# Performance work log

Measured on AMD Instinct MI355X. Metric: run time of the kernel, lower is better.

Reference implementation:

```python
import jax, jax.numpy as jnp
import numpy as np
from jax import lax

B, C, H, W = 32, 384, 56, 56


def setup_inputs() -> dict:
    key = jax.random.key(0)
    k1, k2, k3, k4 = jax.random.split(key, 4)
    x = jax.random.normal(k1, (B, C, H, W), dtype=jnp.float32)
    # positional embedding, trunc_normal(std=0.02) ~ small normal
    pe = 0.02 * jax.random.normal(k2, (1, C, H, 1), dtype=jnp.float32)
    # depthwise conv weight: (out=C, in/groups=1, kH=H, kW=1), PyTorch default init scale
    fan_in = H  # in_channels/groups * kH * kW = 1*H*1
    bound = 1.0 / np.sqrt(fan_in)
    weight = jax.random.uniform(k3, (C, 1, H, 1), dtype=jnp.float32, minval=-bound, maxval=bound)
    bias = jax.random.uniform(k4, (C,), dtype=jnp.float32, minval=-bound, maxval=bound)
    return {"x": x, "pe": pe, "weight": weight, "bias": bias}


def reference(x, pe, weight, bias):
    # PE add
    xp = x + pe  # [B,C,H,W]
    # circular pad along H: concat first H-1 rows at the bottom
    x_cat = jnp.concatenate([xp, xp[:, :, : H - 1, :]], axis=2)  # [B,C,2H-1,W]
    # depthwise conv, kernel (H,1), groups=C -> output [B,C,H,W]
    out = lax.conv_general_dilated(
        x_cat, weight,
        window_strides=(1, 1), padding='VALID',
        dimension_numbers=('NCHW', 'OIHW', 'NCHW'),
        feature_group_count=C,
    )
    return out + bias[None, :, None, None]
```

## Files before the change

kernel.cpp:

```cpp
#include <hip/hip_runtime.h>

#define Cc 384
#define Hh 56
#define Ww 56
#define PLANE (Hh*Ww)
#define NF4 14

typedef short short8 __attribute__((ext_vector_type(8)));
typedef float f32x4  __attribute__((ext_vector_type(4)));
typedef unsigned int u32;
struct __align__(16) f4 { float x, y, z, w; };

__device__ __forceinline__ u32 cvtpk_bf16(float a, float b) {
    u32 d; asm("v_cvt_pk_bf16_f32 %0, %1, %2" : "=v"(d) : "v"(a), "v"(b));
    return d;
}
__device__ __forceinline__ int swz(int w) { return (w ^ (w >> 2)) & 7; }

__global__ __launch_bounds__(256) __attribute__((amdgpu_waves_per_eu(4, 4)))
void parc_kernel(const float* __restrict__ x, const float* __restrict__ pe,
                 const float* __restrict__ wgt, const float* __restrict__ bias,
                 float* __restrict__ out)
{
    __shared__ __align__(16) float Xt[64 * 64];
    __shared__ __align__(16) float Cb[56 * 60];
    __shared__ unsigned short wt2[112];

    const int t  = threadIdx.x;
    const int bc = blockIdx.x;
    const int c  = bc % Cc;

    const float* __restrict__ wc  = wgt + c * Hh;
    const float* __restrict__ pec = pe  + c * Hh;
    const f4* __restrict__ xin = reinterpret_cast<const f4*>(x) + (size_t)bc * (PLANE / 4);

    f4 v0 = xin[t], v1 = xin[t + 256], v2 = xin[t + 512];
    const int r0 = t / NF4, r1 = (t + 256) / NF4, r2 = (t + 512) / NF4;
    const float p0 = pec[r0], p1 = pec[r1], p2 = pec[r2];
    f4 v3; float p3 = 0.f; int r3 = 0;
    if (t < 16) { v3 = xin[t + 768]; r3 = (t + 768) / NF4; p3 = pec[r3]; }

    if (t < 112) {
        const int k = t >= Hh ? t - Hh : t;
        wt2[t] = (unsigned short)(cvtpk_bf16(wc[k], wc[k]) & 0xffffu);
    }

    {
        const int w = t >> 2, j = t & 3, m = 56 + 2 * j;
        const int blk = (m >> 2) ^ swz(w);
        *reinterpret_cast<float2*>((char*)Xt + 256 * w + 16 * blk + 4 * (m & 3))
            = make_float2(0.f, 0.f);
    }

    #define PUT(F, V, R, P) { \
        const int w4_ = (F) % NF4; \
        const int blkb = (R) >> 2, sub = 4 * ((R) & 3); \
        const float a0 = (V).x + (P), a1 = (V).y + (P); \
        const float a2 = (V).z + (P), a3 = (V).w + (P); \
        { const int w = 4 * w4_ + 0; *reinterpret_cast<float*>((char*)Xt + 256*w + 16*(blkb ^ swz(w)) + sub) = a0; } \
        { const int w = 4 * w4_ + 1; *reinterpret_cast<float*>((char*)Xt + 256*w + 16*(blkb ^ swz(w)) + sub) = a1; } \
        { const int w = 4 * w4_ + 2; *reinterpret_cast<float*>((char*)Xt + 256*w + 16*(blkb ^ swz(w)) + sub) = a2; } \
        { const int w = 4 * w4_ + 3; *reinterpret_cast<float*>((char*)Xt + 256*w + 16*(blkb ^ swz(w)) + sub) = a3; } }
    PUT(t,       v0, r0, p0)
    PUT(t + 256, v1, r1, p1)
    PUT(t + 512, v2, r2, p2)
    if (t < 16) PUT(t + 768, v3, r3, p3)
    #undef PUT
    __syncthreads();

    const int l = t & 63, wv = t >> 6, l15 = l & 15, g = l >> 4;

    short8 afr[2];
    #pragma unroll
    for (int step = 0; step < 2; ++step) {
        #pragma unroll
        for (int j = 0; j < 8; ++j) {
            int idx = 32 * step + 8 * g + j - 16 * wv - l15 + 56;
            idx = idx < 0 ? 0 : (idx > 111 ? 111 : idx);
            afr[step][j] = (short)wt2[idx];
        }
    }

    const float bz = bias[c];
    f32x4 acc[4];
    #pragma unroll
    for (int ni = 0; ni < 4; ++ni) acc[ni] = (f32x4){bz, bz, bz, bz};

    #pragma unroll
    for (int step = 0; step < 2; ++step) {
        #pragma unroll
        for (int ni = 0; ni < 4; ++ni) {
            const int w = 16 * ni + l15;
            const int s = swz(w);
            const int blk0 = 2 * g + 8 * step;
            const f32x4 lo = *reinterpret_cast<const f32x4*>((char*)Xt + 256 * w + 16 * (blk0 ^ s));
            const f32x4 hi = *reinterpret_cast<const f32x4*>((char*)Xt + 256 * w + 16 * ((blk0 + 1) ^ s));
            union { u32 d[4]; short8 s8; } bu;
            bu.d[0] = cvtpk_bf16(lo[0], lo[1]);
            bu.d[1] = cvtpk_bf16(lo[2], lo[3]);
            bu.d[2] = cvtpk_bf16(hi[0], hi[1]);
            bu.d[3] = cvtpk_bf16(hi[2], hi[3]);
            acc[ni] = __builtin_amdgcn_mfma_f32_16x16x32_bf16(afr[step], bu.s8, acc[ni], 0, 0, 0);
        }
    }

    #pragma unroll
    for (int ni = 0; ni < 4; ++ni) {
        const int wcol = 16 * ni + l15;
        #pragma unroll
        for (int r = 0; r < 4; ++r) {
            const int h = 16 * wv + 4 * g + r;
            if (h < Hh && wcol < Ww) Cb[60 * h + wcol] = acc[ni][r];
        }
    }
    __syncthreads();

    f4* __restrict__ op = reinterpret_cast<f4*>(out) + (size_t)bc * (PLANE / 4);
    #define GETST(U) { \
        const int rr = (U) / NF4, ww4 = (U) % NF4; \
        op[(U)] = *reinterpret_cast<const f4*>((char*)Cb + 240 * rr + 16 * ww4); }
    GETST(t)
    GETST(t + 256)
    GETST(t + 512)
    if (t < 16) GETST(t + 768)
    #undef GETST
}

extern "C" void kernel_launch(void* const* d_in, const int* in_sizes, int n_in,
                              void* d_out, int out_size, void* d_ws, size_t ws_size,
                              hipStream_t stream) {
    const float* x  = (const float*)d_in[0];
    const float* pe = (const float*)d_in[1];
    const float* w  = (const float*)d_in[2];
    const float* b  = (const float*)d_in[3];
    float* out      = (float*)d_out;

    parc_kernel<<<dim3(32 * Cc), 256, 0, stream>>>(x, pe, w, b, out);
}
```

Baseline: 58.05 us.

## Swap MFMA operand roles: X as A fragment, circulant weight matrix in LDS

Builds the full circulant bf16 weight matrix in shared memory (64x72 padded) so each wave loads its X fragment once and reuses it across four MFMAs, reading weight fragments as vector LDS loads. This replaces the per-element scalar gathers of weight values and the repeated X loads and bf16 conversions per output tile. The output is now written to the staging buffer as 16-byte vector stores instead of scalar stores. In exchange it uses about 9 KB more LDS per block, which may limit occupancy, and does more weight setup work per block.

```diff
diff --git a/kernel.cpp b/kernel.cpp
--- a/kernel.cpp
+++ b/kernel.cpp
@@ -9,6 +9,7 @@
 typedef short short8 __attribute__((ext_vector_type(8)));
 typedef float f32x4  __attribute__((ext_vector_type(4)));
 typedef unsigned int u32;
+typedef u32 u32x4 __attribute__((ext_vector_type(4)));
 struct __align__(16) f4 { float x, y, z, w; };
 
 __device__ __forceinline__ u32 cvtpk_bf16(float a, float b) {
@@ -24,7 +25,7 @@
 {
     __shared__ __align__(16) float Xt[64 * 64];
     __shared__ __align__(16) float Cb[56 * 60];
-    __shared__ unsigned short wt2[112];
+    __shared__ __align__(16) unsigned short Bt[64 * 72];
 
     const int t  = threadIdx.x;
     const int bc = blockIdx.x;
@@ -40,9 +41,21 @@
     f4 v3; float p3 = 0.f; int r3 = 0;
     if (t < 16) { v3 = xin[t + 768]; r3 = (t + 768) / NF4; p3 = pec[r3]; }
 
-    if (t < 112) {
-        const int k = t >= Hh ? t - Hh : t;
-        wt2[t] = (unsigned short)(cvtpk_bf16(wc[k], wc[k]) & 0xffffu);
+    {
+        const int h = t >> 2, mb = (t & 3) << 4;
+        const int j0 = (mb - h + 112) % 56;
+        u32 d[8];
+        #pragma unroll
+        for (int i = 0; i < 8; ++i) {
+            int ja = j0 + 2 * i;     if (ja >= 56) ja -= 56;
+            int jb = j0 + 2 * i + 1; if (jb >= 56) jb -= 56;
+            d[i] = cvtpk_bf16(wc[ja], wc[jb]);
+        }
+        char* p = (char*)Bt + 144 * h + 2 * mb;
+        u32x4 w0 = {d[0], d[1], d[2], d[3]};
+        u32x4 w1 = {d[4], d[5], d[6], d[7]};
+        *reinterpret_cast<u32x4*>(p)      = w0;
+        *reinterpret_cast<u32x4*>(p + 16) = w1;
     }
 
     {
@@ -69,49 +82,37 @@
     __syncthreads();
 
     const int l = t & 63, wv = t >> 6, l15 = l & 15, g = l >> 4;
-
-    short8 afr[2];
-    #pragma unroll
-    for (int step = 0; step < 2; ++step) {
-        #pragma unroll
-        for (int j = 0; j < 8; ++j) {
-            int idx = 32 * step + 8 * g + j - 16 * wv - l15 + 56;
-            idx = idx < 0 ? 0 : (idx > 111 ? 111 : idx);
-            afr[step][j] = (short)wt2[idx];
-        }
-    }
+    const int wA = 16 * wv + l15;
+    const int sA = swz(wA);
 
     const float bz = bias[c];
     f32x4 acc[4];
     #pragma unroll
-    for (int ni = 0; ni < 4; ++ni) acc[ni] = (f32x4){bz, bz, bz, bz};
+    for (int j = 0; j < 4; ++j) acc[j] = (f32x4){bz, bz, bz, bz};
 
     #pragma unroll
     for (int step = 0; step < 2; ++step) {
+        const int blk0 = 2 * g + 8 * step;
+        const f32x4 lo = *reinterpret_cast<const f32x4*>((char*)Xt + 256 * wA + 16 * (blk0 ^ sA));
+        const f32x4 hi = *reinterpret_cast<const f32x4*>((char*)Xt + 256 * wA + 16 * ((blk0 + 1) ^ sA));
+        union { u32 d[4]; short8 s8; } au;
+        au.d[0] = cvtpk_bf16(lo[0], lo[1]);
+        au.d[1] = cvtpk_bf16(lo[2], lo[3]);
+        au.d[2] = cvtpk_bf16(hi[0], hi[1]);
+        au.d[3] = cvtpk_bf16(hi[2], hi[3]);
         #pragma unroll
-        for (int ni = 0; ni < 4; ++ni) {
-            const int w = 16 * ni + l15;
-            const int s = swz(w);
-            const int blk0 = 2 * g + 8 * step;
-            const f32x4 lo = *reinterpret_cast<const f32x4*>((char*)Xt + 256 * w + 16 * (blk0 ^ s));
-            const f32x4 hi = *reinterpret_cast<const f32x4*>((char*)Xt + 256 * w + 16 * ((blk0 + 1) ^ s));
-            union { u32 d[4]; short8 s8; } bu;
-            bu.d[0] = cvtpk_bf16(lo[0], lo[1]);
-            bu.d[1] = cvtpk_bf16(lo[2], lo[3]);
-            bu.d[2] = cvtpk_bf16(hi[0], hi[1]);
-            bu.d[3] = cvtpk_bf16(hi[2], hi[3]);
-            acc[ni] = __builtin_amdgcn_mfma_f32_16x16x32_bf16(afr[step], bu.s8, acc[ni], 0, 0, 0);
+        for (int j = 0; j < 4; ++j) {
+            const short8 bfr = *reinterpret_cast<const short8*>(
+                (char*)Bt + 144 * (16 * j + l15) + 16 * g + 64 * step);
+            acc[j] = __builtin_amdgcn_mfma_f32_16x16x32_bf16(au.s8, bfr, acc[j], 0, 0, 0);
         }
     }
 
     #pragma unroll
-    for (int ni = 0; ni < 4; ++ni) {
-        const int wcol = 16 * ni + l15;
-        #pragma unroll
-        for (int r = 0; r < 4; ++r) {
-            const int h = 16 * wv + 4 * g + r;
-            if (h < Hh && wcol < Ww) Cb[60 * h + wcol] = acc[ni][r];
-        }
+    for (int j = 0; j < 4; ++j) {
+        const int h = 16 * j + l15;
+        if (h < Hh && !(wv == 3 && g >= 2))
+            *reinterpret_cast<f32x4*>((char*)Cb + 240 * h + 64 * wv + 16 * g) = acc[j];
     }
     __syncthreads();
 
```

After: 63.75 us. 9.8% more time.
